# Performance work log

Measured on AMD Instinct MI355X. Metric: run time of the kernel, lower is better.

## Reference

```python
import jax, jax.numpy as jnp
import numpy as np

D = 1024      # d_model
FFN = 4096    # encoder_ffn_dim
INTER = 4096  # intermediate_size (per-expert extra width)
E = 4         # num_experts
S = 3         # num_datasets
NH = 16       # attention heads
HD = D // NH
B = 4
L = 1024


def _ln(x, g, b, eps=1e-5):
    m = x.mean(-1, keepdims=True)
    v = ((x - m) ** 2).mean(-1, keepdims=True)
    return (x - m) / jnp.sqrt(v + eps) * g + b


def setup_inputs() -> dict:
    key = jax.random.key(0)
    keys = iter(jax.random.split(key, 32))

    def w(shape):
        return jax.random.normal(next(keys), shape, dtype=jnp.float32) * 0.02

    inp = {}
    inp["hidden_states"] = jax.random.normal(next(keys), (B, L, D), dtype=jnp.float32)
    inp["attention_mask"] = jnp.zeros((B, 1, L, L), jnp.float32)
    inp["layer_head_mask"] = jnp.ones((NH,), jnp.float32)
    inp["idxes"] = jax.random.randint(next(keys), (B,), 0, S, dtype=jnp.int32)
    for name, shape in [("q_w", (D, D)), ("k_w", (D, D)), ("v_w", (D, D)), ("o_w", (D, D)),
                        ("fc1_w", (FFN, D)), ("fc2_w", (D, FFN)),
                        ("exp_fc1_w", (E, INTER, D)), ("exp_fc2_w", (E, D, INTER)),
                        ("gate_w", (S, E, D))]:
        inp[name] = w(shape)
    for name, shape in [("q_b", (D,)), ("k_b", (D,)), ("v_b", (D,)), ("o_b", (D,)),
                        ("fc1_b", (FFN,)), ("fc2_b", (D,)),
                        ("exp_fc1_b", (E, INTER)), ("gate_b", (S, E))]:
        inp[name] = jnp.zeros(shape, jnp.float32)
    inp["ln1_g"] = jnp.ones((D,), jnp.float32)
    inp["ln1_b"] = jnp.zeros((D,), jnp.float32)
    inp["ln2_g"] = jnp.ones((D,), jnp.float32)
    inp["ln2_b"] = jnp.zeros((D,), jnp.float32)
    return inp


def reference(hidden_states, attention_mask, layer_head_mask, idxes,
              q_w, q_b, k_w, k_b, v_w, v_b, o_w, o_b,
              ln1_g, ln1_b, fc1_w, fc1_b, fc2_w, fc2_b,
              exp_fc1_w, exp_fc1_b, exp_fc2_w, gate_w, gate_b,
              ln2_g, ln2_b):
    Bb, Ll, Dm = hidden_states.shape
    residual = hidden_states
    scale = HD ** -0.5

    def heads(t):  # [B,L,D] -> [B,NH,L,HD]
        return t.reshape(Bb, Ll, NH, HD).transpose(0, 2, 1, 3)

    q = heads(hidden_states @ q_w.T + q_b) * scale
    k = heads(hidden_states @ k_w.T + k_b)
    v = heads(hidden_states @ v_w.T + v_b)
    scores = jnp.einsum('bhqd,bhkd->bhqk', q, k) + attention_mask  # [B,NH,L,L]
    probs = jax.nn.softmax(scores, axis=-1) * layer_head_mask[None, :, None, None]
    attn = jnp.einsum('bhqk,bhkd->bhqd', probs, v).transpose(0, 2, 1, 3).reshape(Bb, Ll, Dm)
    h = residual + attn @ o_w.T + o_b
    h = _ln(h, ln1_g, ln1_b)

    # --- MoE feed-forward (token-level top-1 routing, per-dataset gates) ---
    x = h.reshape(-1, Dm)                 # [T, D]
    ds = jnp.repeat(idxes, Ll)            # [T] dataset id per token
    Wg = gate_w[ds]                       # [T, E, D]
    logits = jnp.einsum('td,ted->te', x, Wg) + gate_b[ds]
    gp = jax.nn.softmax(logits, axis=-1)
    gate_value = gp.max(-1)               # [T]
    gate_idx = gp.argmax(-1)              # [T]

    out = jnp.zeros_like(x)
    for e in range(E):  # small fixed expert count
        W1 = jnp.concatenate([fc1_w, exp_fc1_w[e]], axis=0)     # [FFN+INTER, D]
        b1 = jnp.concatenate([fc1_b, exp_fc1_b[e]], axis=0)
        W2 = jnp.concatenate([fc2_w, exp_fc2_w[e]], axis=1)     # [D, FFN+INTER]
        hh = jax.nn.gelu(x @ W1.T + b1, approximate=False)
        y = hh @ W2.T + fc2_b
        y = _ln(x + y, ln2_g, ln2_b)
        out = out + jnp.where(gate_idx == e, gate_value, 0.0)[:, None] * y
    return out.reshape(Bb, Ll, Dm)
```

## Files before the change

kernel.cpp:

```cpp
#include <hip/hip_runtime.h>
#include <cstdint>
#include <cstddef>

#define DEV __device__ __forceinline__

typedef __bf16 bf16;
typedef __bf16 bf16x8 __attribute__((ext_vector_type(8)));
typedef __bf16 bf16x4v __attribute__((ext_vector_type(4)));
typedef float  f32x4  __attribute__((ext_vector_type(4)));
typedef float  f32x16 __attribute__((ext_vector_type(16)));
typedef unsigned int uint4v __attribute__((ext_vector_type(4)));

static constexpr int D_   = 1024;
static constexpr int FFN_ = 4096;
static constexpr int NH_  = 16;
static constexpr int HD_  = 64;
static constexpr int SEQ_ = 1024;
static constexpr int T_   = 4 * SEQ_;
static constexpr float L2E_ = 1.4426950408889634f;

DEV float gelu_f(float x) {
  float g2 = x * fmaf(-0.102944f, x * x, -2.302212f);
  return x * __builtin_amdgcn_rcpf(1.f + exp2f(g2));
}

DEV unsigned pk2h(float a, float b) {
  unsigned ua = __builtin_bit_cast(unsigned short, (bf16)a);
  unsigned ub = __builtin_bit_cast(unsigned short, (bf16)b);
  return ua | (ub << 16);
}
DEV unsigned pk2l(float a, float b) {
  bf16 ha = (bf16)a, hb = (bf16)b;
  unsigned ua = __builtin_bit_cast(unsigned short, (bf16)(a - (float)ha));
  unsigned ub = __builtin_bit_cast(unsigned short, (bf16)(b - (float)hb));
  return ua | (ub << 16);
}
DEV bf16x8 mk8(unsigned w0, unsigned w1, unsigned w2, unsigned w3) {
  uint4v v = {w0, w1, w2, w3};
  return __builtin_bit_cast(bf16x8, v);
}

__global__ __launch_bounds__(256) void k_cvt4(const float* __restrict__ a, const float* __restrict__ b,
                                              const float* __restrict__ c, const float* __restrict__ d,
                                              bf16* __restrict__ dst)
{
  size_t i = ((size_t)blockIdx.x * 256 + threadIdx.x) * 4;
  constexpr size_t M1 = 4ull << 20, M2 = 20ull << 20, M3 = 24ull << 20, M4 = 40ull << 20;
  const float* src; size_t si;
  if (i < M1)      { src = a; si = i; }
  else if (i < M2) { src = b; si = i - M1; }
  else if (i < M3) { src = c; si = i - M2; }
  else if (i < M4) { src = d; si = i - M3; }
  else return;
  float4 v = *(const float4*)(src + si);
  bf16x4v o;
  o[0] = (bf16)v.x; o[1] = (bf16)v.y; o[2] = (bf16)v.z; o[3] = (bf16)v.w;
  *(bf16x4v*)(dst + i) = o;
}

__global__ __launch_bounds__(256) void k_cvt_split_all(
    const float* __restrict__ h, const float* __restrict__ qw, const float* __restrict__ kw,
    const float* __restrict__ vw, const float* __restrict__ ow, bf16* __restrict__ out)
{
  int i = (blockIdx.x * 256 + threadIdx.x) * 4;
  if (i >= (8 << 20)) return;
  int seg = i >> 20;
  const float* src; int si;
  if (seg < 4)       { src = h;  si = i; }
  else if (seg == 4) { src = qw; si = i - (4 << 20); }
  else if (seg == 5) { src = kw; si = i - (5 << 20); }
  else if (seg == 6) { src = vw; si = i - (6 << 20); }
  else               { src = ow; si = i - (7 << 20); }
  float4 v = *(const float4*)(src + si);
  int r = i >> 10, c = i & 1023;
  bf16* base = out + (size_t)r * 2048 + c;
  float xs[4] = {v.x, v.y, v.z, v.w};
  #pragma unroll
  for (int j = 0; j < 4; ++j) {
    float x = xs[j];
    bf16 hi = (bf16)x;
    bf16 lo = (bf16)(x - (float)hi);
    base[j]        = hi;
    base[1024 + j] = lo;
  }
}

enum { EPI_QKV = 0, EPI_OPROJ, EPI_FF1, EPI_FF2 };

DEV int map_akt(int kt, bool split) { return split ? (kt < 64 ? kt : kt - 64) : kt; }
DEV int map_bkt(int kt, bool split) { return split ? (kt < 32 ? kt : kt - 32) : kt; }

template<int EPI, bool SPLIT, int TM, int TN, bool NEWSYNC>
__global__ __launch_bounds__(256)
void k_gemm(const bf16* __restrict__ A, const bf16* __restrict__ Bw,
            const float* __restrict__ bias, const float* __restrict__ bias2,
            const float* __restrict__ bias3, const float* __restrict__ resid,
            float* __restrict__ outF, bf16* __restrict__ outB,
            bf16* __restrict__ o2, bf16* __restrict__ o3,
            const int* __restrict__ perm, const int* __restrict__ seg,
            int Kphys, int nk, float scale)
{
  constexpr bool FUSED = (EPI == EPI_FF1 || EPI == EPI_FF2);
  constexpr int  NCOL  = (EPI == EPI_FF1) ? 4096 : 1024;
  constexpr int  SBX   = 4096 / TM;
  constexpr int  MF    = (TN == 128) ? (TM / 32) : (TM / 64);
  constexpr int  AISS  = TM / 64;
  constexpr int  BISS  = TN / 64;

  __shared__ __align__(16) bf16 sA[2][TM * 32];
  __shared__ __align__(16) bf16 sB[2][TN * 32];

  const int tid  = threadIdx.x;
  const int lane = tid & 63;
  const int w    = tid >> 6;
  const int lr   = lane & 15, kg = lane >> 4;
  const int wmBase = (TN == 128) ? (w >> 1) * (TM / 2) : w * (TM / 4);
  const int wnBase = (TN == 128) ? (w & 1) * 64 : 0;

  int bx, by, kz = 0;
  if constexpr (EPI == EPI_FF2) {
    int wk = (blockIdx.x & 7) * 136 + (blockIdx.x >> 3);
    kz = wk / 544; int r2 = wk % 544;
    bx = r2 >> 3; by = r2 & 7;
  } else {
    bx = blockIdx.x; by = blockIdx.y; kz = blockIdx.z;
  }
  const int ktBase = (EPI == EPI_OPROJ || EPI == EPI_FF2) ? kz * nk : 0;

  const bool expertBlk = FUSED && (bx >= SBX);
  int e = 0;
  if (FUSED && expertBlk) { int r0 = (bx - SBX) * TM; while (e < 3 && r0 >= seg[e + 1]) e++; }
  const bf16* Bp = Bw + (expertBlk ? (size_t)(e + 1) * NCOL * Kphys : 0);

  const bf16* aSrc[AISS]; const bf16* bSrc[BISS];
  #pragma unroll
  for (int i = 0; i < AISS; ++i) {
    int c = tid + i * 256;
    int koff = (c & 3) * 8;
    if (EPI == EPI_FF1 && expertBlk) {
      int pr = perm[(bx - SBX) * TM + (c >> 2)];
      aSrc[i] = A + (size_t)(pr < 0 ? 0 : pr) * Kphys + koff;
    } else {
      aSrc[i] = A + (size_t)(bx * TM + (c >> 2)) * Kphys + koff;
    }
  }
  #pragma unroll
  for (int i = 0; i < BISS; ++i) {
    int c = tid + i * 256;
    int koff = (c & 3) * 8;
    bSrc[i] = Bp + (size_t)(by * TN + (c >> 2)) * Kphys + koff;
  }

  f32x4 acc[MF][4] = {};

  {
    int ak0 = map_akt(ktBase, SPLIT), bk0 = map_bkt(ktBase, SPLIT);
    #pragma unroll
    for (int i = 0; i < AISS; ++i)
      __builtin_amdgcn_global_load_lds((const void*)(aSrc[i] + (size_t)ak0 * 32),
                                       (void*)((char*)sA[0] + (tid + i * 256) * 16), 16, 0, 0);
    #pragma unroll
    for (int i = 0; i < BISS; ++i)
      __builtin_amdgcn_global_load_lds((const void*)(bSrc[i] + (size_t)bk0 * 32),
                                       (void*)((char*)sB[0] + (tid + i * 256) * 16), 16, 0, 0);
  }
  __syncthreads();

  for (int kt = 0; kt < nk; ++kt) {
    const int cur = kt & 1;
    if (kt + 1 < nk) {
      int ak = map_akt(ktBase + kt + 1, SPLIT), bk = map_bkt(ktBase + kt + 1, SPLIT);
      #pragma unroll
      for (int i = 0; i < AISS; ++i)
        __builtin_amdgcn_global_load_lds((const void*)(aSrc[i] + (size_t)ak * 32),
                                         (void*)((char*)sA[cur ^ 1] + (tid + i * 256) * 16), 16, 0, 0);
      #pragma unroll
      for (int i = 0; i < BISS; ++i)
        __builtin_amdgcn_global_load_lds((const void*)(bSrc[i] + (size_t)bk * 32),
                                         (void*)((char*)sB[cur ^ 1] + (tid + i * 256) * 16), 16, 0, 0);
      if constexpr (NEWSYNC) {
        asm volatile("s_waitcnt vmcnt(4)" ::: "memory");
      }
    } else if constexpr (NEWSYNC) {
      asm volatile("s_waitcnt vmcnt(0)" ::: "memory");
    }
    if constexpr (NEWSYNC) {
      asm volatile("s_barrier" ::: "memory");
    }
    bf16x8 af[MF], bfr[4];
    #pragma unroll
    for (int m = 0; m < MF; ++m)
      af[m] = *(const bf16x8*)&sA[cur][(wmBase + m * 16 + lr) * 32 + kg * 8];
    #pragma unroll
    for (int n = 0; n < 4; ++n)
      bfr[n] = *(const bf16x8*)&sB[cur][(wnBase + n * 16 + lr) * 32 + kg * 8];
    #pragma unroll
    for (int m = 0; m < MF; ++m)
      #pragma unroll
      for (int n = 0; n < 4; ++n)
        acc[m][n] = __builtin_amdgcn_mfma_f32_16x16x32_bf16(af[m], bfr[n], acc[m][n], 0, 0, 0);
    if constexpr (NEWSYNC) {
      asm volatile("s_barrier" ::: "memory");
    } else {
      __syncthreads();
    }
  }

  #pragma unroll
  for (int m = 0; m < MF; ++m) {
    #pragma unroll
    for (int n = 0; n < 4; ++n) {
      int gc = by * TN + wnBase + n * 16 + lr;
      #pragma unroll
      for (int r = 0; r < 4; ++r) {
        int row = bx * TM + wmBase + m * 16 + kg * 4 + r;
        float v = acc[m][n][r];
        if constexpr (EPI == EPI_QKV) {
          const int which = by >> 3;
          const int wcol = gc & 1023;
          int bq = row >> 10, li = row & 1023, hh = wcol >> 6, d = wcol & 63;
          if (which == 0) {
            float y = (v + bias[wcol]) * scale;
            bf16* base = outB + ((size_t)(bq * NH_ + hh) * SEQ_ + li) * 128 + d;
            bf16 hi = (bf16)y, lo = (bf16)(y - (float)hi);
            base[0] = hi; base[64] = lo;
          } else if (which == 1) {
            float y = v + bias2[wcol];
            bf16* base = o2 + ((size_t)(bq * NH_ + hh) * SEQ_ + li) * 128 + d;
            bf16 hi = (bf16)y, lo = (bf16)(y - (float)hi);
            base[0] = hi; base[64] = lo;
          } else {
            float y = v + bias3[wcol];
            bf16* base = o3 + ((size_t)(bq * NH_ + hh) * HD_ + d) * 2048 + li;
            bf16 hi = (bf16)y, lo = (bf16)(y - (float)hi);
            base[0] = hi; base[1024] = lo;
          }
        } else if constexpr (EPI == EPI_OPROJ) {
          outF[((size_t)kz * 4096 + row) * 1024 + gc] = v;
        } else if constexpr (EPI == EPI_FF1) {
          float y = v + (expertBlk ? bias2[e * 4096 + gc] : bias[gc]);
          outB[(size_t)row * 4096 + gc] = (bf16)gelu_f(y);
        } else if constexpr (EPI == EPI_FF2) {
          o2[((size_t)kz * 8704 + row) * 1024 + gc] = (bf16)v;
        }
      }
    }
  }
}

__global__ __launch_bounds__(256)
void k_attn(const bf16* __restrict__ q2, const bf16* __restrict__ k2,
            const bf16* __restrict__ vT2, const float* __restrict__ mask,
            const float* __restrict__ lhm, bf16* __restrict__ ctx2)
{
  const int blk = (blockIdx.x & 7) * 64 + (blockIdx.x >> 3);
  const int bh = blk >> 3, qb = blk & 7;
  const int tid = threadIdx.x;
  const int w = tid >> 6, lane = tid & 63;
  const int lq = lane & 31, hi = lane >> 5;
  const int b = bh >> 4, h = bh & 15;
  const int q0 = qb * 128 + w * 32;

  __shared__ __align__(16) bf16 sK[2][4096];
  __shared__ __align__(16) bf16 sV[2][4096];

  const bf16* qp = q2 + ((size_t)bh * SEQ_ + q0 + lq) * 128;
  bf16x8 qh[4], ql[4];
  #pragma unroll
  for (int s = 0; s < 4; ++s) {
    qh[s] = *(const bf16x8*)(qp + s * 16 + hi * 8);
    ql[s] = *(const bf16x8*)(qp + 64 + s * 16 + hi * 8);
  }

  const bf16* kp = k2 + (size_t)bh * SEQ_ * 128;
  const bf16* vp = vT2 + (size_t)bh * HD_ * 2048;
  const float* mp = mask + ((size_t)b * SEQ_ + q0 + lq) * SEQ_;

  auto stage = [&](int buf, int kb) {
    #pragma unroll
    for (int i = 0; i < 2; ++i) {
      int c = i * 256 + w * 64 + lane;
      int cs = c ^ ((c >> 4) & 7);
      __builtin_amdgcn_global_load_lds((const void*)(kp + (size_t)kb * 128 + cs * 8),
                                       (void*)&sK[buf][(size_t)(i * 256 + w * 64) * 8], 16, 0, 0);
      int d = c >> 3, p = (c & 7) ^ (d & 7);
      const bf16* vsrc = vp + (size_t)d * 2048 + (p < 4 ? kb + p * 8 : 1024 + kb + (p - 4) * 8);
      __builtin_amdgcn_global_load_lds((const void*)vsrc,
                                       (void*)&sV[buf][(size_t)(i * 256 + w * 64) * 8], 16, 0, 0);
    }
  };

  float m_run = -1e30f, l_run = 0.f;
  f32x16 ot[2] = {};

  float4 mreg[4];
  #pragma unroll
  for (int r4 = 0; r4 < 4; ++r4)
    mreg[r4] = *(const float4*)(mp + 8 * r4 + 4 * hi);

  stage(0, 0);
  __syncthreads();

  for (int kc = 0; kc < SEQ_ / 32; ++kc) {
    const int kb = kc * 32;
    const int cur = kc & 1;
    if (kc + 1 < SEQ_ / 32) stage(cur ^ 1, kb + 32);

    const char* kbase = (const char*)sK[cur];
    const char* vbase = (const char*)sV[cur];

    f32x16 st = {};
    __builtin_amdgcn_s_setprio(1);
    #pragma unroll
    for (int s = 0; s < 4; ++s) {
      int gh = s * 2 + hi, gl = 8 + s * 2 + hi;
      bf16x8 kh = *(const bf16x8*)(kbase + lq * 256 + ((gh ^ (lq & 7)) << 4));
      bf16x8 kl = *(const bf16x8*)(kbase + lq * 256 + ((gl ^ (lq & 7)) << 4));
      st = __builtin_amdgcn_mfma_f32_32x32x16_bf16(kh, qh[s], st, 0, 0, 0);
      st = __builtin_amdgcn_mfma_f32_32x32x16_bf16(kh, ql[s], st, 0, 0, 0);
      st = __builtin_amdgcn_mfma_f32_32x32x16_bf16(kl, qh[s], st, 0, 0, 0);
    }
    __builtin_amdgcn_s_setprio(0);
    #pragma unroll
    for (int reg = 0; reg < 16; ++reg)
      st[reg] = fmaf(((const float*)&mreg[reg >> 2])[reg & 3], L2E_, st[reg]);
    if (kc + 1 < SEQ_ / 32) {
      #pragma unroll
      for (int r4 = 0; r4 < 4; ++r4)
        mreg[r4] = *(const float4*)(mp + kb + 32 + 8 * r4 + 4 * hi);
    }

    float cm = st[0];
    #pragma unroll
    for (int reg = 1; reg < 16; ++reg) cm = fmaxf(cm, st[reg]);
    cm = fmaxf(cm, __shfl_xor(cm, 32, 64));
    float mnew = fmaxf(m_run, cm);
    float alpha = exp2f(m_run - mnew);
    float p[16];
    #pragma unroll
    for (int reg = 0; reg < 16; ++reg) p[reg] = exp2f(st[reg] - mnew);
    float rs = p[0];
    #pragma unroll
    for (int reg = 1; reg < 16; ++reg) rs += p[reg];
    rs += __shfl_xor(rs, 32, 64);
    l_run = l_run * alpha + rs; m_run = mnew;
    #pragma unroll
    for (int i = 0; i < 16; ++i) { ot[0][i] *= alpha; ot[1][i] *= alpha; }

    unsigned hA0 = pk2h(p[0], p[1]),  hA1 = pk2h(p[2], p[3]);
    unsigned hB0 = pk2h(p[4], p[5]),  hB1 = pk2h(p[6], p[7]);
    unsigned hC0 = pk2h(p[8], p[9]),  hC1 = pk2h(p[10], p[11]);
    unsigned hD0 = pk2h(p[12], p[13]), hD1 = pk2h(p[14], p[15]);
    unsigned lA0 = pk2l(p[0], p[1]),  lA1 = pk2l(p[2], p[3]);
    unsigned lB0 = pk2l(p[4], p[5]),  lB1 = pk2l(p[6], p[7]);
    unsigned lC0 = pk2l(p[8], p[9]),  lC1 = pk2l(p[10], p[11]);
    unsigned lD0 = pk2l(p[12], p[13]), lD1 = pk2l(p[14], p[15]);
    unsigned x0 = (unsigned)__shfl_xor((int)(hi ? hA0 : hB0), 32, 64);
    unsigned x1 = (unsigned)__shfl_xor((int)(hi ? hA1 : hB1), 32, 64);
    unsigned x2 = (unsigned)__shfl_xor((int)(hi ? hC0 : hD0), 32, 64);
    unsigned x3 = (unsigned)__shfl_xor((int)(hi ? hC1 : hD1), 32, 64);
    unsigned y0 = (unsigned)__shfl_xor((int)(hi ? lA0 : lB0), 32, 64);
    unsigned y1 = (unsigned)__shfl_xor((int)(hi ? lA1 : lB1), 32, 64);
    unsigned y2 = (unsigned)__shfl_xor((int)(hi ? lC0 : lD0), 32, 64);
    unsigned y3 = (unsigned)__shfl_xor((int)(hi ? lC1 : lD1), 32, 64);
    bf16x8 pb0h = hi ? mk8(x0, x1, hB0, hB1) : mk8(hA0, hA1, x0, x1);
    bf16x8 pb1h = hi ? mk8(x2, x3, hD0, hD1) : mk8(hC0, hC1, x2, x3);
    bf16x8 pb0l = hi ? mk8(y0, y1, lB0, lB1) : mk8(lA0, lA1, y0, y1);
    bf16x8 pb1l = hi ? mk8(y2, y3, lD0, lD1) : mk8(lC0, lC1, y2, y3);

    __builtin_amdgcn_s_setprio(1);
    #pragma unroll
    for (int ks = 0; ks < 2; ++ks) {
      bf16x8 pbh = ks ? pb1h : pb0h;
      bf16x8 pbl = ks ? pb1l : pb0l;
      #pragma unroll
      for (int t = 0; t < 2; ++t) {
        int row = t * 32 + lq;
        int gh = ks * 2 + hi, gl = 4 + ks * 2 + hi;
        bf16x8 vh = *(const bf16x8*)(vbase + row * 128 + ((gh ^ (row & 7)) << 4));
        bf16x8 vl = *(const bf16x8*)(vbase + row * 128 + ((gl ^ (row & 7)) << 4));
        ot[t] = __builtin_amdgcn_mfma_f32_32x32x16_bf16(vh, pbh, ot[t], 0, 0, 0);
        ot[t] = __builtin_amdgcn_mfma_f32_32x32x16_bf16(vh, pbl, ot[t], 0, 0, 0);
        ot[t] = __builtin_amdgcn_mfma_f32_32x32x16_bf16(vl, pbh, ot[t], 0, 0, 0);
      }
    }
    __builtin_amdgcn_s_setprio(0);

    __syncthreads();
  }

  const float rln = lhm[h] / l_run;
  bf16* base = ctx2 + ((size_t)b * SEQ_ + q0 + lq) * 2048;
  #pragma unroll
  for (int t = 0; t < 2; ++t)
    #pragma unroll
    for (int reg = 0; reg < 16; ++reg) {
      int d = (reg & 3) + 8 * (reg >> 2) + 4 * hi + 32 * t;
      int col = h * HD_ + d;
      float y = ot[t][reg] * rln;
      bf16 yh = (bf16)y, yl = (bf16)(y - (float)yh);
      base[col] = yh; base[1024 + col] = yl;
    }
}

DEV float blockReduceSum(float v, int tid, float* sm)
{
  #pragma unroll
  for (int d = 1; d < 64; d <<= 1) v += __shfl_xor(v, d, 64);
  if ((tid & 63) == 0) sm[tid >> 6] = v;
  __syncthreads();
  float r = sm[0] + sm[1] + sm[2] + sm[3];
  __syncthreads();
  return r;
}

__global__ __launch_bounds__(256)
void k_ln1gate(const float* __restrict__ resid, const float* __restrict__ Pp, const float* __restrict__ ob,
               const float* __restrict__ gam, const float* __restrict__ bet,
               const float* __restrict__ gw, const float* __restrict__ gb, const int* __restrict__ idxes,
               float* __restrict__ h, bf16* __restrict__ hb,
               float* __restrict__ gv, int* __restrict__ gi)
{
  __shared__ float sm[4];
  __shared__ float red[4][4];
  int t = blockIdx.x, tid = threadIdx.x;
  constexpr size_t CH = 4096ull * 1024ull;
  float4 rv = *(const float4*)(resid + (size_t)t * 1024 + tid * 4);
  float4 p0 = *(const float4*)(Pp + (size_t)t * 1024 + tid * 4);
  float4 p1 = *(const float4*)(Pp + CH + (size_t)t * 1024 + tid * 4);
  float4 bo = *(const float4*)(ob + tid * 4);
  float z0 = rv.x + p0.x + p1.x + bo.x;
  float z1 = rv.y + p0.y + p1.y + bo.y;
  float z2 = rv.z + p0.z + p1.z + bo.z;
  float z3 = rv.w + p0.w + p1.w + bo.w;
  float mean = blockReduceSum(z0 + z1 + z2 + z3, tid, sm) * (1.f / 1024.f);
  float d0 = z0 - mean, d1 = z1 - mean, d2 = z2 - mean, d3 = z3 - mean;
  float var = blockReduceSum(d0*d0 + d1*d1 + d2*d2 + d3*d3, tid, sm) * (1.f / 1024.f);
  float inv = rsqrtf(var + 1e-5f);
  float4 g4 = *(const float4*)(gam + tid * 4);
  float4 b4 = *(const float4*)(bet + tid * 4);
  float y0 = d0 * inv * g4.x + b4.x, y1 = d1 * inv * g4.y + b4.y;
  float y2 = d2 * inv * g4.z + b4.z, y3 = d3 * inv * g4.w + b4.w;
  float4 yo; yo.x = y0; yo.y = y1; yo.z = y2; yo.w = y3;
  *(float4*)(h + (size_t)t * 1024 + tid * 4) = yo;
  bf16x4v hv; hv[0] = (bf16)y0; hv[1] = (bf16)y1; hv[2] = (bf16)y2; hv[3] = (bf16)y3;
  *(bf16x4v*)(hb + (size_t)t * 1024 + tid * 4) = hv;

  int ds = idxes[t >> 10];
  const float* wg = gw + (size_t)ds * 4096;
  float a[4];
  #pragma unroll
  for (int e = 0; e < 4; ++e) {
    float4 wv = *(const float4*)(wg + e * 1024 + tid * 4);
    a[e] = y0 * wv.x + y1 * wv.y + y2 * wv.z + y3 * wv.w;
  }
  int lane = tid & 63, wid = tid >> 6;
  #pragma unroll
  for (int e = 0; e < 4; ++e) {
    float vv = a[e];
    #pragma unroll
    for (int d = 1; d < 64; d <<= 1) vv += __shfl_xor(vv, d, 64);
    if (lane == 0) red[wid][e] = vv;
  }
  __syncthreads();
  if (tid == 0) {
    float lg[4];
    #pragma unroll
    for (int e = 0; e < 4; ++e) lg[e] = red[0][e] + red[1][e] + red[2][e] + red[3][e] + gb[ds * 4 + e];
    int best = 0; float bv = lg[0];
    #pragma unroll
    for (int e = 1; e < 4; ++e) if (lg[e] > bv) { bv = lg[e]; best = e; }
    float se = 0.f;
    #pragma unroll
    for (int e = 0; e < 4; ++e) se += expf(lg[e] - bv);
    gv[t] = 1.f / se;
    gi[t] = best;
  }
}

__global__ __launch_bounds__(1024)
void k_route_all(const int* __restrict__ gi, int* __restrict__ meta,
                 int* __restrict__ perm, int* __restrict__ inv)
{
  __shared__ int cnt[4], seg[5], cur[4];
  int tid = threadIdx.x;
  if (tid < 4) { cnt[tid] = 0; cur[tid] = 0; }
  __syncthreads();
  #pragma unroll
  for (int k = 0; k < 4; ++k) atomicAdd(&cnt[gi[tid + k * 1024]], 1);
  #pragma unroll
  for (int k = 0; k < 5; ++k) { int i = tid + k * 1024; if (i < 4608) perm[i] = -1; }
  __syncthreads();
  if (tid == 0) {
    int s = 0;
    #pragma unroll
    for (int e = 0; e < 4; ++e) { seg[e] = s; s += (cnt[e] + 127) & ~127; }
    seg[4] = s;
    #pragma unroll
    for (int e = 0; e < 5; ++e) meta[8 + e] = seg[e];
  }
  __syncthreads();
  #pragma unroll
  for (int k = 0; k < 4; ++k) {
    int t = tid + k * 1024;
    int e = gi[t];
    int p = atomicAdd(&cur[e], 1);
    int rowp = seg[e] + p;
    perm[rowp] = t;
    inv[t] = rowp;
  }
}

__global__ __launch_bounds__(256)
void k_final(const float* __restrict__ h, const bf16* __restrict__ P,
             const float* __restrict__ b2, const float* __restrict__ gam,
             const float* __restrict__ bet, const float* __restrict__ gv,
             const int* __restrict__ inv, float* __restrict__ out)
{
  __shared__ float sm[4];
  int t = blockIdx.x, tid = threadIdx.x;
  constexpr size_t CH = 8704ull * 1024ull;
  int er = 4096 + inv[t];
  bf16x4v q0 = *(const bf16x4v*)(P + (size_t)t * 1024 + tid * 4);
  bf16x4v q1 = *(const bf16x4v*)(P + CH + (size_t)t * 1024 + tid * 4);
  bf16x4v q2 = *(const bf16x4v*)(P + (size_t)er * 1024 + tid * 4);
  bf16x4v q3 = *(const bf16x4v*)(P + CH + (size_t)er * 1024 + tid * 4);
  float4 a = *(const float4*)(h + (size_t)t * 1024 + tid * 4);
  float4 bb = *(const float4*)(b2 + tid * 4);
  float z0 = a.x + (float)q0[0] + (float)q1[0] + (float)q2[0] + (float)q3[0] + bb.x;
  float z1 = a.y + (float)q0[1] + (float)q1[1] + (float)q2[1] + (float)q3[1] + bb.y;
  float z2 = a.z + (float)q0[2] + (float)q1[2] + (float)q2[2] + (float)q3[2] + bb.z;
  float z3 = a.w + (float)q0[3] + (float)q1[3] + (float)q2[3] + (float)q3[3] + bb.w;
  float mean = blockReduceSum(z0 + z1 + z2 + z3, tid, sm) * (1.f / 1024.f);
  float d0 = z0 - mean, d1 = z1 - mean, d2 = z2 - mean, d3 = z3 - mean;
  float var = blockReduceSum(d0*d0 + d1*d1 + d2*d2 + d3*d3, tid, sm) * (1.f / 1024.f);
  float invd = rsqrtf(var + 1e-5f);
  float4 g4 = *(const float4*)(gam + tid * 4);
  float4 b4 = *(const float4*)(bet + tid * 4);
  float gval = gv[t];
  float4 r;
  r.x = gval * (d0 * invd * g4.x + b4.x);
  r.y = gval * (d1 * invd * g4.y + b4.y);
  r.z = gval * (d2 * invd * g4.z + b4.z);
  r.w = gval * (d3 * invd * g4.w + b4.w);
  *(float4*)(out + (size_t)t * 1024 + tid * 4) = r;
}

extern "C" void kernel_launch(void* const* d_in, const int* in_sizes, int n_in,
                              void* d_out, int out_size, void* d_ws, size_t ws_size,
                              hipStream_t stream)
{
  const float* hidden = (const float*)d_in[0];
  const float* mask   = (const float*)d_in[1];
  const float* lhm    = (const float*)d_in[2];
  const int*   idxes  = (const int*)d_in[3];
  const float* qw = (const float*)d_in[4];
  const float* kw = (const float*)d_in[5];
  const float* vw = (const float*)d_in[6];
  const float* ow = (const float*)d_in[7];
  const float* fc1w  = (const float*)d_in[8];
  const float* fc2w  = (const float*)d_in[9];
  const float* efc1w = (const float*)d_in[10];
  const float* efc2w = (const float*)d_in[11];
  const float* gatew = (const float*)d_in[12];
  const float* qb = (const float*)d_in[13];
  const float* kb = (const float*)d_in[14];
  const float* vb = (const float*)d_in[15];
  const float* ob = (const float*)d_in[16];
  const float* fc1b  = (const float*)d_in[17];
  const float* fc2b  = (const float*)d_in[18];
  const float* efc1b = (const float*)d_in[19];
  const float* gateb = (const float*)d_in[20];
  const float* ln1g = (const float*)d_in[21];
  const float* ln1b = (const float*)d_in[22];
  const float* ln2g = (const float*)d_in[23];
  const float* ln2b = (const float*)d_in[24];
  float* out = (float*)d_out;
  char* ws = (char*)d_ws;

  constexpr size_t MB = 1024ull * 1024ull;
  constexpr size_t O_H    = 0;
  constexpr size_t O_HBF  = O_H + 16 * MB;
  constexpr size_t O_GV   = O_HBF + 8 * MB;
  constexpr size_t O_GI   = O_GV + 16 * 1024;
  constexpr size_t O_PERM = O_GI + 16 * 1024;
  constexpr size_t O_META = O_PERM + 18432;
  constexpr size_t O_INV  = O_META + 256;
  constexpr size_t O_U    = (O_INV + 16384 + 255) & ~255ull;
  constexpr size_t O_X2   = O_U;
  constexpr size_t O_WQ2  = O_X2 + 16 * MB;
  constexpr size_t O_Q2   = O_WQ2 + 16 * MB;
  constexpr size_t O_K2   = O_Q2 + 16 * MB;
  constexpr size_t O_VT2  = O_K2 + 16 * MB;
  constexpr size_t O_CTX2 = O_VT2 + 16 * MB;
  constexpr size_t O_HPRE = O_CTX2 + 16 * MB;
  constexpr size_t O_WO2  = O_WQ2 + 12 * MB;
  constexpr size_t O_W1B  = O_U;
  constexpr size_t O_WE1B = O_W1B + 8 * MB;
  constexpr size_t O_W2B  = O_WE1B + 32 * MB;
  constexpr size_t O_WE2B = O_W2B + 8 * MB;
  constexpr size_t O_HHS  = O_WE2B + 32 * MB;
  constexpr size_t O_HHE  = O_HHS + 32 * MB;
  constexpr size_t O_P    = O_HHE + 36 * MB;
  (void)ws_size; (void)in_sizes; (void)n_in; (void)out_size;

  dim3 blk(256);
  k_cvt_split_all<<<8192, 256, 0, stream>>>(hidden, qw, kw, vw, ow, (bf16*)(ws + O_X2));

  const float qscale = 0.125f * L2E_;
  k_gemm<EPI_QKV, true, 128, 128, true><<<dim3(32, 24), blk, 0, stream>>>(
      (bf16*)(ws + O_X2), (bf16*)(ws + O_WQ2), qb, kb, vb, nullptr,
      nullptr, (bf16*)(ws + O_Q2), (bf16*)(ws + O_K2), (bf16*)(ws + O_VT2),
      nullptr, nullptr, 2048, 96, qscale);

  k_attn<<<512, 256, 0, stream>>>((bf16*)(ws + O_Q2), (bf16*)(ws + O_K2), (bf16*)(ws + O_VT2),
                                  mask, lhm, (bf16*)(ws + O_CTX2));

  k_gemm<EPI_OPROJ, true, 128, 64, true><<<dim3(32, 16, 2), blk, 0, stream>>>(
      (bf16*)(ws + O_CTX2), (bf16*)(ws + O_WO2), nullptr, nullptr, nullptr, nullptr,
      (float*)(ws + O_HPRE), nullptr, nullptr, nullptr, nullptr, nullptr, 2048, 48, 1.0f);
  k_ln1gate<<<4096, 256, 0, stream>>>(hidden, (float*)(ws + O_HPRE), ob, ln1g, ln1b,
                                      gatew, gateb, idxes,
                                      (float*)(ws + O_H), (bf16*)(ws + O_HBF),
                                      (float*)(ws + O_GV), (int*)(ws + O_GI));

  k_cvt4<<<40960, 256, 0, stream>>>(fc1w, efc1w, fc2w, efc2w, (bf16*)(ws + O_W1B));
  k_route_all<<<1, 1024, 0, stream>>>((int*)(ws + O_GI), (int*)(ws + O_META),
                                      (int*)(ws + O_PERM), (int*)(ws + O_INV));

  k_gemm<EPI_FF1, false, 128, 128, true><<<dim3(68, 32), blk, 0, stream>>>(
      (bf16*)(ws + O_HBF), (bf16*)(ws + O_W1B), fc1b, efc1b, nullptr, nullptr,
      nullptr, (bf16*)(ws + O_HHS), nullptr, nullptr,
      (int*)(ws + O_PERM), (int*)(ws + O_META) + 8, 1024, 32, 1.0f);
  k_gemm<EPI_FF2, false, 128, 128, true><<<dim3(1088), blk, 0, stream>>>(
      (bf16*)(ws + O_HHS), (bf16*)(ws + O_W2B), nullptr, nullptr, nullptr, nullptr,
      nullptr, nullptr, (bf16*)(ws + O_P), nullptr,
      nullptr, (int*)(ws + O_META) + 8, 4096, 64, 1.0f);

  k_final<<<4096, 256, 0, stream>>>((float*)(ws + O_H), (bf16*)(ws + O_P), fc2b, ln2g, ln2b,
                                    (float*)(ws + O_GV), (int*)(ws + O_INV), out);
}
```

Before: 531.3 us.

## Fuse FFN weight conversion into attention kernel launch to overlap with attention

New measurement: 555.3 us. +4.5%, slower.

```diff
diff --git a/kernel.cpp b/kernel.cpp
--- a/kernel.cpp
+++ b/kernel.cpp
@@ -38,24 +38,6 @@
 DEV bf16x8 mk8(unsigned w0, unsigned w1, unsigned w2, unsigned w3) {
   uint4v v = {w0, w1, w2, w3};
   return __builtin_bit_cast(bf16x8, v);
-}
-
-__global__ __launch_bounds__(256) void k_cvt4(const float* __restrict__ a, const float* __restrict__ b,
-                                              const float* __restrict__ c, const float* __restrict__ d,
-                                              bf16* __restrict__ dst)
-{
-  size_t i = ((size_t)blockIdx.x * 256 + threadIdx.x) * 4;
-  constexpr size_t M1 = 4ull << 20, M2 = 20ull << 20, M3 = 24ull << 20, M4 = 40ull << 20;
-  const float* src; size_t si;
-  if (i < M1)      { src = a; si = i; }
-  else if (i < M2) { src = b; si = i - M1; }
-  else if (i < M3) { src = c; si = i - M2; }
-  else if (i < M4) { src = d; si = i - M3; }
-  else return;
-  float4 v = *(const float4*)(src + si);
-  bf16x4v o;
-  o[0] = (bf16)v.x; o[1] = (bf16)v.y; o[2] = (bf16)v.z; o[3] = (bf16)v.w;
-  *(bf16x4v*)(dst + i) = o;
 }
 
 __global__ __launch_bounds__(256) void k_cvt_split_all(
@@ -249,10 +231,32 @@
 }
 
 __global__ __launch_bounds__(256)
-void k_attn(const bf16* __restrict__ q2, const bf16* __restrict__ k2,
-            const bf16* __restrict__ vT2, const float* __restrict__ mask,
-            const float* __restrict__ lhm, bf16* __restrict__ ctx2)
-{
+void k_attn_cvt(const bf16* __restrict__ q2, const bf16* __restrict__ k2,
+                const bf16* __restrict__ vT2, const float* __restrict__ mask,
+                const float* __restrict__ lhm, bf16* __restrict__ ctx2,
+                const float* __restrict__ wa, const float* __restrict__ wb,
+                const float* __restrict__ wc, const float* __restrict__ wd,
+                bf16* __restrict__ wdst)
+{
+  __shared__ __align__(16) bf16 sK[2][4096];
+  __shared__ __align__(16) bf16 sV[2][4096];
+
+  if (blockIdx.x >= 512) {
+    size_t i = ((size_t)(blockIdx.x - 512) * 256 + threadIdx.x) * 4;
+    constexpr size_t M1 = 4ull << 20, M2 = 20ull << 20, M3 = 24ull << 20, M4 = 40ull << 20;
+    const float* src; size_t si;
+    if (i < M1)      { src = wa; si = i; }
+    else if (i < M2) { src = wb; si = i - M1; }
+    else if (i < M3) { src = wc; si = i - M2; }
+    else if (i < M4) { src = wd; si = i - M3; }
+    else return;
+    float4 v = *(const float4*)(src + si);
+    bf16x4v o;
+    o[0] = (bf16)v.x; o[1] = (bf16)v.y; o[2] = (bf16)v.z; o[3] = (bf16)v.w;
+    *(bf16x4v*)(wdst + i) = o;
+    return;
+  }
+
   const int blk = (blockIdx.x & 7) * 64 + (blockIdx.x >> 3);
   const int bh = blk >> 3, qb = blk & 7;
   const int tid = threadIdx.x;
@@ -260,9 +264,6 @@
   const int lq = lane & 31, hi = lane >> 5;
   const int b = bh >> 4, h = bh & 15;
   const int q0 = qb * 128 + w * 32;
-
-  __shared__ __align__(16) bf16 sK[2][4096];
-  __shared__ __align__(16) bf16 sV[2][4096];
 
   const bf16* qp = q2 + ((size_t)bh * SEQ_ + q0 + lq) * 128;
   bf16x8 qh[4], ql[4];
@@ -587,21 +588,22 @@
   constexpr size_t O_META = O_PERM + 18432;
   constexpr size_t O_INV  = O_META + 256;
   constexpr size_t O_U    = (O_INV + 16384 + 255) & ~255ull;
-  constexpr size_t O_X2   = O_U;
-  constexpr size_t O_WQ2  = O_X2 + 16 * MB;
-  constexpr size_t O_Q2   = O_WQ2 + 16 * MB;
-  constexpr size_t O_K2   = O_Q2 + 16 * MB;
-  constexpr size_t O_VT2  = O_K2 + 16 * MB;
-  constexpr size_t O_CTX2 = O_VT2 + 16 * MB;
-  constexpr size_t O_HPRE = O_CTX2 + 16 * MB;
-  constexpr size_t O_WO2  = O_WQ2 + 12 * MB;
   constexpr size_t O_W1B  = O_U;
   constexpr size_t O_WE1B = O_W1B + 8 * MB;
   constexpr size_t O_W2B  = O_WE1B + 32 * MB;
   constexpr size_t O_WE2B = O_W2B + 8 * MB;
-  constexpr size_t O_HHS  = O_WE2B + 32 * MB;
-  constexpr size_t O_HHE  = O_HHS + 32 * MB;
-  constexpr size_t O_P    = O_HHE + 36 * MB;
+  constexpr size_t O_A    = O_U + 80 * MB;
+  constexpr size_t O_X2   = O_A;
+  constexpr size_t O_WQ2  = O_A + 16 * MB;
+  constexpr size_t O_WO2  = O_WQ2 + 12 * MB;
+  constexpr size_t O_Q2   = O_A + 32 * MB;
+  constexpr size_t O_K2   = O_A + 48 * MB;
+  constexpr size_t O_VT2  = O_A + 64 * MB;
+  constexpr size_t O_CTX2 = O_A + 80 * MB;
+  constexpr size_t O_HPRE = O_Q2;
+  constexpr size_t O_HHS  = O_A;
+  constexpr size_t O_HHE  = O_A + 32 * MB;
+  constexpr size_t O_P    = O_A + 68 * MB;
   (void)ws_size; (void)in_sizes; (void)n_in; (void)out_size;
 
   dim3 blk(256);
@@ -613,8 +615,9 @@
       nullptr, (bf16*)(ws + O_Q2), (bf16*)(ws + O_K2), (bf16*)(ws + O_VT2),
       nullptr, nullptr, 2048, 96, qscale);
 
-  k_attn<<<512, 256, 0, stream>>>((bf16*)(ws + O_Q2), (bf16*)(ws + O_K2), (bf16*)(ws + O_VT2),
-                                  mask, lhm, (bf16*)(ws + O_CTX2));
+  k_attn_cvt<<<41472, 256, 0, stream>>>((bf16*)(ws + O_Q2), (bf16*)(ws + O_K2), (bf16*)(ws + O_VT2),
+                                        mask, lhm, (bf16*)(ws + O_CTX2),
+                                        fc1w, efc1w, fc2w, efc2w, (bf16*)(ws + O_W1B));
 
   k_gemm<EPI_OPROJ, true, 128, 64, true><<<dim3(32, 16, 2), blk, 0, stream>>>(
       (bf16*)(ws + O_CTX2), (bf16*)(ws + O_WO2), nullptr, nullptr, nullptr, nullptr,
@@ -624,7 +627,6 @@
                                       (float*)(ws + O_H), (bf16*)(ws + O_HBF),
                                       (float*)(ws + O_GV), (int*)(ws + O_GI));
 
-  k_cvt4<<<40960, 256, 0, stream>>>(fc1w, efc1w, fc2w, efc2w, (bf16*)(ws + O_W1B));
   k_route_all<<<1, 1024, 0, stream>>>((int*)(ws + O_GI), (int*)(ws + O_META),
                                       (int*)(ws + O_PERM), (int*)(ws + O_INV));
 
```
